# Kernel tuning notes

Hardware: AMD Instinct MI355X
Metric: run time of the kernel (lower is better)

## Reference

```python
import jax, jax.numpy as jnp
import numpy as np

EPS = 1e-6
WINDOW = 1024  # config.sliding_window; mask: causal AND (q_idx - kv_idx < WINDOW)


def rms_norm(x, w=None):
    y = x * jax.lax.rsqrt(jnp.mean(jnp.square(x), axis=-1, keepdims=True) + EPS)
    return y * w if w is not None else y


def rotate_half(x):
    x1, x2 = jnp.split(x, 2, axis=-1)
    return jnp.concatenate([-x2, x1], axis=-1)


def apply_rope(x, cos, sin):
    # x: [B,S,H,D], cos/sin: [B,S,D] -> unsqueeze head dim (rotary_dim == D, x_pass empty)
    cos = cos[:, :, None, :]
    sin = sin[:, :, None, :]
    return x * cos + rotate_half(x) * sin


def setup_inputs() -> dict:
    key = jax.random.key(0)
    ks = jax.random.split(key, 8)
    B, S, HID, NH, NKV, D = 1, 2048, 2560, 8, 4, 256
    scale = 0.02
    hidden_states = jax.random.normal(ks[0], (B, S, HID), dtype=jnp.float32)
    wq = jax.random.normal(ks[1], (HID, NH * D), dtype=jnp.float32) * scale
    wk = jax.random.normal(ks[2], (HID, NKV * D), dtype=jnp.float32) * scale
    wv = jax.random.normal(ks[3], (HID, NKV * D), dtype=jnp.float32) * scale
    wo = jax.random.normal(ks[4], (NH * D, HID), dtype=jnp.float32) * scale
    q_norm_w = jnp.ones((D,), dtype=jnp.float32)
    k_norm_w = jnp.ones((D,), dtype=jnp.float32)
    # standard RoPE tables, rotary_dim = head_dim
    pos = jnp.arange(S, dtype=jnp.float32)
    inv_freq = 1.0 / (10000.0 ** (jnp.arange(0, D, 2, dtype=jnp.float32) / D))
    freqs = pos[:, None] * inv_freq[None, :]           # [S, D/2]
    emb = jnp.concatenate([freqs, freqs], axis=-1)     # [S, D]
    cos = jnp.cos(emb)[None]                           # [1, S, D]
    sin = jnp.sin(emb)[None]
    return dict(hidden_states=hidden_states, cos=cos, sin=sin,
                wq=wq, wk=wk, wv=wv, wo=wo,
                q_norm_w=q_norm_w, k_norm_w=k_norm_w)


def reference(hidden_states, cos, sin, wq, wk, wv, wo, q_norm_w, k_norm_w):
    B, S, _ = hidden_states.shape
    D = q_norm_w.shape[0]
    # projections -> [B,S,H,D]
    q = (hidden_states @ wq).reshape(B, S, -1, D)
    k = (hidden_states @ wk).reshape(B, S, -1, D)
    v = (hidden_states @ wv).reshape(B, S, -1, D)
    # QK-norm then RoPE (v gets non-affine RMSNorm)
    q = apply_rope(rms_norm(q, q_norm_w), cos, sin)
    k = apply_rope(rms_norm(k, k_norm_w), cos, sin)
    v = rms_norm(v)
    NH, NKV = q.shape[2], k.shape[2]
    rep = NH // NKV  # GQA: repeat KV heads
    k = jnp.repeat(k, rep, axis=2)
    v = jnp.repeat(v, rep, axis=2)
    # attention with scale=1.0 (QK-norm replaces 1/sqrt(d))
    scores = jnp.einsum('bqhd,bkhd->bhqk', q, k)
    qi = jnp.arange(S)[:, None]
    ki = jnp.arange(S)[None, :]
    mask = (ki <= qi) & (qi - ki < WINDOW)  # causal sliding window
    scores = jnp.where(mask[None, None], scores, -jnp.inf)
    attn = jax.nn.softmax(scores, axis=-1)
    out = jnp.einsum('bhqk,bkhd->bqhd', attn, v).reshape(B, S, -1)
    return out @ wo
```

## Files before the change

kernel.cpp:

```cpp
#include <hip/hip_runtime.h>
#include <hip/hip_bf16.h>
#include <math.h>

#define S_LEN 2048
#define HID 2560
#define NH 8
#define NKV 4
#define HD 256
#define WINDOW 1024

typedef short short8 __attribute__((ext_vector_type(8)));
typedef short short4_t __attribute__((ext_vector_type(4)));
typedef float f32x4 __attribute__((ext_vector_type(4)));
typedef float float4_t __attribute__((ext_vector_type(4)));

__device__ __forceinline__ short bf16_rne(float x) {
  unsigned u = __float_as_uint(x);
  return (short)((u + 0x7FFFu + ((u >> 16) & 1u)) >> 16);
}
__device__ __forceinline__ void split2(float x, short &h, short &l) {
  unsigned u = __float_as_uint(x);
  unsigned hb = (u + 0x7FFFu + ((u >> 16) & 1u)) & 0xFFFF0000u;
  h = (short)(hb >> 16);
  float r = x - __uint_as_float(hb);
  l = bf16_rne(r);
}

__device__ __forceinline__ void gload16(const short* g, short* l) {
  __builtin_amdgcn_global_load_lds(
      (const __attribute__((address_space(1))) void*)g,
      (__attribute__((address_space(3))) void*)l, 16, 0, 0);
}

#define SWZ(g, r) ((((g) ^ ((r) & 7))) * 8)
template <int MODE>
__device__ __forceinline__ void gemm_body(
    const short* __restrict__ Ah, const short* __restrict__ Al,
    const short* __restrict__ Bh, const short* __restrict__ Bl,
    float* __restrict__ C, int K, int ldc, int m0, int n0, int tid,
    short (*__restrict__ Ahs)[64], short (*__restrict__ Als)[64],
    short (*__restrict__ Bhs)[64], short (*__restrict__ Bls)[64]) {
  constexpr bool USE_AL = (MODE & 1) != 0;
  constexpr bool USE_BL = (MODE & 2) != 0;
  const int wv = tid >> 6, lane = tid & 63;
  const int wm = (wv >> 1) * 32, wn = (wv & 1) * 64;
  const int quad = lane >> 4, col = lane & 15;
  const int lr = lane >> 3;
  const size_t lgofs = (size_t)(((lane & 7) ^ lr)) * 8;
  const size_t aBase = (size_t)(m0 + lr) * K + lgofs;
  const size_t bBase = (size_t)(n0 + lr) * K + lgofs;

  f32x4 acc[2][4];
#pragma unroll
  for (int i = 0; i < 2; i++)
#pragma unroll
    for (int j = 0; j < 4; j++) acc[i][j] = (f32x4){0.f, 0.f, 0.f, 0.f};

  for (int k0 = 0; k0 < K; k0 += 64) {
#pragma unroll
    for (int c = wv; c < 8; c += 4) {
      const size_t go = aBase + (size_t)c * 8 * K + k0;
      gload16(Ah + go, &Ahs[c * 8][0]);
      if (USE_AL) gload16(Al + go, &Als[c * 8][0]);
    }
#pragma unroll
    for (int c = wv; c < 16; c += 4) {
      const size_t go = bBase + (size_t)c * 8 * K + k0;
      gload16(Bh + go, &Bhs[c * 8][0]);
      if (USE_BL) gload16(Bl + go, &Bls[c * 8][0]);
    }
    __syncthreads();
#pragma unroll
    for (int ks = 0; ks < 2; ks++) {
      const int g = ks * 4 + quad;
      short8 afh[2], afl[2], bfh[4], bfl[4];
#pragma unroll
      for (int i = 0; i < 2; i++) {
        int ar = wm + i * 16 + col;
        afh[i] = *reinterpret_cast<const short8*>(&Ahs[ar][SWZ(g, ar)]);
        if (USE_AL)
          afl[i] = *reinterpret_cast<const short8*>(&Als[ar][SWZ(g, ar)]);
      }
#pragma unroll
      for (int j = 0; j < 4; j++) {
        int br = wn + j * 16 + col;
        bfh[j] = *reinterpret_cast<const short8*>(&Bhs[br][SWZ(g, br)]);
        if (USE_BL)
          bfl[j] = *reinterpret_cast<const short8*>(&Bls[br][SWZ(g, br)]);
      }
#pragma unroll
      for (int i = 0; i < 2; i++)
#pragma unroll
        for (int j = 0; j < 4; j++) {
          acc[i][j] = __builtin_amdgcn_mfma_f32_16x16x32_bf16(afh[i], bfh[j], acc[i][j], 0, 0, 0);
          if (USE_BL)
            acc[i][j] = __builtin_amdgcn_mfma_f32_16x16x32_bf16(afh[i], bfl[j], acc[i][j], 0, 0, 0);
          if (USE_AL)
            acc[i][j] = __builtin_amdgcn_mfma_f32_16x16x32_bf16(afl[i], bfh[j], acc[i][j], 0, 0, 0);
        }
    }
    __syncthreads();
  }
#pragma unroll
  for (int i = 0; i < 2; i++)
#pragma unroll
    for (int j = 0; j < 4; j++)
#pragma unroll
      for (int r = 0; r < 4; r++)
        C[(size_t)(m0 + wm + i * 16 + quad * 4 + r) * ldc + n0 + wn + j * 16 + col] =
            acc[i][j][r];
}

template <int MODE>
__global__ __launch_bounds__(256, 3)
void gemm_presplit(const short* __restrict__ Ah, const short* __restrict__ Al,
                   const short* __restrict__ Bh, const short* __restrict__ Bl,
                   float* __restrict__ C, int K, int ldc) {
  __shared__ short Ahs[64][64];
  __shared__ short Als[(MODE & 1) ? 64 : 1][64];
  __shared__ short Bhs[128][64];
  __shared__ short Bls[(MODE & 2) ? 128 : 1][64];
  gemm_body<MODE>(Ah, Al, Bh, Bl, C, K, ldc, blockIdx.y * 64, blockIdx.x * 128,
                  threadIdx.x, Ahs, Als, Bhs, Bls);
}

__global__ __launch_bounds__(256, 3)
void gemm_qkv(const short* __restrict__ Ah, const short* __restrict__ Al,
              const short* __restrict__ qkvTh, const short* __restrict__ qkvTl,
              float* __restrict__ Cqkv) {
  __shared__ short Ahs[64][64];
  __shared__ short Als[64][64];
  __shared__ short Bhs[128][64];
  __shared__ short Bls[128][64];
  const int b = blockIdx.x;
  if (b < 768) {
    gemm_body<3>(Ah, Al, qkvTh, qkvTl, Cqkv, HID, 4096, (b / 24) * 64,
                 (b % 24) * 128, threadIdx.x, Ahs, Als, Bhs, Bls);
  } else {
    const int t = b - 768;
    gemm_body<2>(Ah, Al, qkvTh + (size_t)3072 * HID, qkvTl + (size_t)3072 * HID,
                 Cqkv + 3072, HID, 4096, (t / 8) * 64, (t % 8) * 128,
                 threadIdx.x, Ahs, Als, Bhs, Bls);
  }
}

__device__ __forceinline__ void wsplitT_body(const float* __restrict__ W,
                                             short* __restrict__ WTh,
                                             short* __restrict__ WTl,
                                             int KW, int NW, int n_ofs,
                                             int k0, int n0, int tid,
                                             float (*T)[65]) {
  const int r = tid >> 4, c4 = (tid & 15) * 4;
#pragma unroll
  for (int p = 0; p < 4; p++) {
    float4_t v = *reinterpret_cast<const float4_t*>(
        &W[(size_t)(k0 + r + p * 16) * NW + n0 + c4]);
#pragma unroll
    for (int e = 0; e < 4; e++) T[r + p * 16][c4 + e] = v[e];
  }
  __syncthreads();
  const int gk = tid & 7;
#pragma unroll
  for (int pass = 0; pass < 2; pass++) {
    const int n_loc = (tid >> 3) + pass * 32;
    short8 hv, lv;
#pragma unroll
    for (int e = 0; e < 8; e++) {
      short hh, ll;
      split2(T[gk * 8 + e][n_loc], hh, ll);
      hv[e] = hh; lv[e] = ll;
    }
    size_t base = (size_t)(n_ofs + n0 + n_loc) * KW + k0 + gk * 8;
    *reinterpret_cast<short8*>(WTh + base) = hv;
    *reinterpret_cast<short8*>(WTl + base) = lv;
  }
}

__global__ __launch_bounds__(256)
void prep_kernel(const float* __restrict__ hs, const float* __restrict__ wq,
                 const float* __restrict__ wk, const float* __restrict__ wv,
                 const float* __restrict__ wo, short* __restrict__ Ah,
                 short* __restrict__ Al, short* __restrict__ qkvTh,
                 short* __restrict__ qkvTl, short* __restrict__ woTh,
                 short* __restrict__ woTl) {
  __shared__ float T[64][65];
  const int bx = blockIdx.x;
  const int tid = threadIdx.x;
  if (bx < 5120) {
    const int i = bx * 256 + tid;
    float4_t v = reinterpret_cast<const float4_t*>(hs)[i];
    short4_t h, l;
#pragma unroll
    for (int e = 0; e < 4; e++) {
      short hh, ll;
      split2(v[e], hh, ll);
      h[e] = hh; l[e] = ll;
    }
    reinterpret_cast<short4_t*>(Ah)[i] = h;
    reinterpret_cast<short4_t*>(Al)[i] = l;
  } else if (bx < 6400) {
    const int local = bx - 5120;
    wsplitT_body(wq, qkvTh, qkvTl, HID, 2048, 0, (local % 40) * 64,
                 (local / 40) * 64, tid, T);
  } else if (bx < 7040) {
    const int local = bx - 6400;
    wsplitT_body(wk, qkvTh, qkvTl, HID, 1024, 2048, (local % 40) * 64,
                 (local / 40) * 64, tid, T);
  } else if (bx < 7680) {
    const int local = bx - 7040;
    wsplitT_body(wv, qkvTh, qkvTl, HID, 1024, 3072, (local % 40) * 64,
                 (local / 40) * 64, tid, T);
  } else {
    const int local = bx - 7680;
    wsplitT_body(wo, woTh, woTl, 2048, HID, 0, (local % 32) * 64,
                 (local / 32) * 64, tid, T);
  }
}

__global__ __launch_bounds__(256)
void norm_kernel(const float* __restrict__ Cqkv, const float* __restrict__ kw,
                 const float* __restrict__ cosb, const float* __restrict__ sinb,
                 short* __restrict__ kh, short* __restrict__ kl,
                 short* __restrict__ vtb) {
  const int u = blockIdx.x & 7;
  const int sq = blockIdx.x >> 3;
  const int d = threadIdx.x;
  const int colbase = (u < 4) ? 2048 + u * HD : 3072 + (u - 4) * HD;
  const size_t idx = (size_t)sq * 4096 + colbase + d;
  float x = Cqkv[idx];
  float v = x * x;
#pragma unroll
  for (int off = 32; off; off >>= 1) v += __shfl_down(v, off);
  __shared__ float red[4];
  __shared__ float sscale;
  __shared__ float nb[HD];
  if ((d & 63) == 0) red[d >> 6] = v;
  __syncthreads();
  if (d == 0)
    sscale = rsqrtf((red[0] + red[1] + red[2] + red[3]) * (1.0f / HD) + 1e-6f);
  __syncthreads();
  if (u < 4) {
    float n = x * sscale * kw[d];
    nb[d] = n;
    __syncthreads();
    float other = (d < HD / 2) ? -nb[d + HD / 2] : nb[d - HD / 2];
    n = n * cosb[(size_t)sq * HD + d] + other * sinb[(size_t)sq * HD + d];
    short hh, ll;
    split2(n, hh, ll);
    const size_t b = ((size_t)sq * NKV + u) * HD + d;
    kh[b] = hh;
    kl[b] = ll;
  } else {
    vtb[((size_t)(u - 4) * HD + d) * S_LEN + sq] = bf16_rne(x * sscale);
  }
}

#define KSW(g, r) (((g) ^ ((r) & 7)) * 8)
#define VSW(g, d) ((((g) + ((d) >> 1)) & 3) * 8)
__global__ __launch_bounds__(256, 2)
void flash_attn2(const float* __restrict__ qn, int qrs,
                 const float* __restrict__ qw, const float* __restrict__ cosb,
                 const float* __restrict__ sinb,
                 const short* __restrict__ kh, const short* __restrict__ kl,
                 const short* __restrict__ vtb, float* __restrict__ oA,
                 float* __restrict__ oB, float* __restrict__ mlA,
                 float* __restrict__ mlB) {
  __shared__ short Kh[32][256], Kl[32][256];
  __shared__ short Vb[256][32];
  __shared__ short Ps[64][32];
  const int qt = blockIdx.x, h = blockIdx.y, sp = blockIdx.z;
  const int kvh = h >> 1;
  const int q0 = qt * 64;
  const int tid = threadIdx.x;
  const int w = tid >> 6, lane = tid & 63;
  const int quad = lane >> 4, col = lane & 15;
  float* oOut = sp ? oB : oA;
  float* mlOut = sp ? mlB : mlA;
  short8 qh[8], ql[8];
  {
    const int sq = q0 + w * 16 + col;
    const float* qrow = qn + (size_t)sq * qrs + h * HD;
    float xq[8][8];
    float ssum = 0.f;
#pragma unroll
    for (int s8 = 0; s8 < 8; s8++) {
      const int d0 = s8 * 32 + quad * 8;
      float4_t a = *reinterpret_cast<const float4_t*>(qrow + d0);
      float4_t b = *reinterpret_cast<const float4_t*>(qrow + d0 + 4);
#pragma unroll
      for (int e = 0; e < 4; e++) {
        xq[s8][e] = a[e];
        xq[s8][4 + e] = b[e];
        ssum += a[e] * a[e] + b[e] * b[e];
      }
    }
    ssum += __shfl_xor(ssum, 16);
    ssum += __shfl_xor(ssum, 32);
    const float scale = rsqrtf(ssum * (1.0f / HD) + 1e-6f);
#pragma unroll
    for (int s8 = 0; s8 < 8; s8++) {
      const int d0 = s8 * 32 + quad * 8;
      float4_t w0 = *reinterpret_cast<const float4_t*>(qw + d0);
      float4_t w1 = *reinterpret_cast<const float4_t*>(qw + d0 + 4);
#pragma unroll
      for (int e = 0; e < 4; e++) {
        xq[s8][e] *= scale * w0[e];
        xq[s8][4 + e] *= scale * w1[e];
      }
    }
    const float* crow = cosb + (size_t)sq * HD;
    const float* srow = sinb + (size_t)sq * HD;
#pragma unroll
    for (int s8 = 0; s8 < 8; s8++) {
      const int d0 = s8 * 32 + quad * 8;
      float4_t c0 = *reinterpret_cast<const float4_t*>(crow + d0);
      float4_t c1 = *reinterpret_cast<const float4_t*>(crow + d0 + 4);
      float4_t s0 = *reinterpret_cast<const float4_t*>(srow + d0);
      float4_t s1 = *reinterpret_cast<const float4_t*>(srow + d0 + 4);
      const float sgn = (s8 < 4) ? -1.f : 1.f;
      const int pp = s8 ^ 4;
#pragma unroll
      for (int e = 0; e < 4; e++) {
        short hh, ll;
        split2(xq[s8][e] * c0[e] + sgn * xq[pp][e] * s0[e], hh, ll);
        qh[s8][e] = hh; ql[s8][e] = ll;
        split2(xq[s8][4 + e] * c1[e] + sgn * xq[pp][4 + e] * s1[e], hh, ll);
        qh[s8][4 + e] = hh; ql[s8][4 + e] = ll;
      }
    }
  }
  f32x4 o[16];
#pragma unroll
  for (int i = 0; i < 16; i++) o[i] = (f32x4){0.f, 0.f, 0.f, 0.f};
  float m_r[4] = {-INFINITY, -INFINITY, -INFINITY, -INFINITY};
  float l_r[4] = {0.f, 0.f, 0.f, 0.f};
  const int lo_t = (q0 > 1023) ? ((q0 - 1023) >> 5) : 0;
  const int hi_t = (q0 + 63) >> 5;
  const int halfn = (hi_t - lo_t + 2) >> 1;
  const int t0 = sp ? (lo_t + halfn) : lo_t;
  const int t1 = sp ? hi_t : (lo_t + halfn - 1);
  for (int kt = t0; kt <= t1; kt++) {
    const int kt0 = kt << 5;
    __syncthreads();
#pragma unroll
    for (int i = 0; i < 4; i++) {
      int idx = tid + i * 256;
      int row = idx >> 5, g = idx & 31;
      size_t gofs = ((size_t)(kt0 + row) * NKV + kvh) * HD + g * 8;
      *reinterpret_cast<short8*>(&Kh[row][KSW(g, row)]) =
          *reinterpret_cast<const short8*>(kh + gofs);
      *reinterpret_cast<short8*>(&Kl[row][KSW(g, row)]) =
          *reinterpret_cast<const short8*>(kl + gofs);
    }
#pragma unroll
    for (int i = 0; i < 4; i++) {
      int idx = tid + i * 256;
      int d = idx >> 2, g = idx & 3;
      *reinterpret_cast<short8*>(&Vb[d][VSW(g, d)]) =
          *reinterpret_cast<const short8*>(
              vtb + ((size_t)kvh * HD + d) * S_LEN + kt0 + g * 8);
    }
    __syncthreads();
    f32x4 sc[2];
    sc[0] = (f32x4){0.f, 0.f, 0.f, 0.f};
    sc[1] = (f32x4){0.f, 0.f, 0.f, 0.f};
#pragma unroll
    for (int s8 = 0; s8 < 8; s8++) {
#pragma unroll
      for (int nt = 0; nt < 2; nt++) {
        const int br = nt * 16 + col;
        const short8 bh = *reinterpret_cast<const short8*>(
            &Kh[br][KSW(s8 * 4 + quad, br)]);
        const short8 bl = *reinterpret_cast<const short8*>(
            &Kl[br][KSW(s8 * 4 + quad, br)]);
        sc[nt] = __builtin_amdgcn_mfma_f32_16x16x32_bf16(qh[s8], bh, sc[nt], 0, 0, 0);
        sc[nt] = __builtin_amdgcn_mfma_f32_16x16x32_bf16(qh[s8], bl, sc[nt], 0, 0, 0);
        sc[nt] = __builtin_amdgcn_mfma_f32_16x16x32_bf16(ql[s8], bh, sc[nt], 0, 0, 0);
      }
    }
#pragma unroll
    for (int r = 0; r < 4; r++) {
      const int q_abs = q0 + w * 16 + quad * 4 + r;
      const int prow = w * 16 + quad * 4 + r;
#pragma unroll
      for (int nt = 0; nt < 2; nt++) {
        int k_abs = kt0 + nt * 16 + col;
        bool valid = (k_abs <= q_abs) && (q_abs - k_abs < WINDOW);
        if (!valid) sc[nt][r] = -INFINITY;
      }
      float mx = fmaxf(sc[0][r], sc[1][r]);
      mx = fmaxf(mx, __shfl_xor(mx, 1));
      mx = fmaxf(mx, __shfl_xor(mx, 2));
      mx = fmaxf(mx, __shfl_xor(mx, 4));
      mx = fmaxf(mx, __shfl_xor(mx, 8));
      float mn = fmaxf(m_r[r], mx);
      float alpha = (mn == -INFINITY) ? 1.f : __expf(m_r[r] - mn);
      m_r[r] = mn;
      float rsum = 0.f;
#pragma unroll
      for (int nt = 0; nt < 2; nt++) {
        float s = sc[nt][r];
        float e = (s == -INFINITY) ? 0.f : __expf(s - mn);
        rsum += e;
        int ge = nt * 2 + (col >> 3);
        Ps[prow][VSW(ge, prow) + (col & 7)] = bf16_rne(e);
      }
      rsum += __shfl_xor(rsum, 1);
      rsum += __shfl_xor(rsum, 2);
      rsum += __shfl_xor(rsum, 4);
      rsum += __shfl_xor(rsum, 8);
      l_r[r] = l_r[r] * alpha + rsum;
#pragma unroll
      for (int nt2 = 0; nt2 < 16; nt2++) o[nt2][r] *= alpha;
    }
    __syncthreads();
    {
      const int prow = w * 16 + col;
      const short8 pa = *reinterpret_cast<const short8*>(&Ps[prow][VSW(quad, prow)]);
#pragma unroll
      for (int nt = 0; nt < 16; nt++) {
        const int vr = nt * 16 + col;
        const short8 vb = *reinterpret_cast<const short8*>(&Vb[vr][VSW(quad, vr)]);
        o[nt] = __builtin_amdgcn_mfma_f32_16x16x32_bf16(pa, vb, o[nt], 0, 0, 0);
      }
    }
  }
#pragma unroll
  for (int r = 0; r < 4; r++) {
    const int row = q0 + w * 16 + quad * 4 + r;
    const size_t base = ((size_t)row * NH + h) * HD;
#pragma unroll
    for (int nt = 0; nt < 16; nt++) oOut[base + nt * 16 + col] = o[nt][r];
    if (col == 0) {
      mlOut[((size_t)row * NH + h) * 2] = m_r[r];
      mlOut[((size_t)row * NH + h) * 2 + 1] = l_r[r];
    }
  }
}

__global__ __launch_bounds__(256)
void combine_kernel(const float* __restrict__ oA, const float* __restrict__ oB,
                    const float* __restrict__ mlA, const float* __restrict__ mlB,
                    short* __restrict__ ctxh) {
  const int idx = blockIdx.x;
  const int d = threadIdx.x;
  const float mA = mlA[(size_t)idx * 2], lA = mlA[(size_t)idx * 2 + 1];
  const float mB = mlB[(size_t)idx * 2], lB = mlB[(size_t)idx * 2 + 1];
  const float m = fmaxf(mA, mB);
  const float eA = (mA == -INFINITY) ? 0.f : __expf(mA - m);
  const float eB = (mB == -INFINITY) ? 0.f : __expf(mB - m);
  const float inv = 1.0f / (eA * lA + eB * lB);
  const size_t b = (size_t)idx * HD + d;
  ctxh[b] = bf16_rne((eA * oA[b] + eB * oB[b]) * inv);
}

extern "C" void kernel_launch(void* const* d_in, const int* in_sizes, int n_in,
                              void* d_out, int out_size, void* d_ws, size_t ws_size,
                              hipStream_t stream) {
  const float* hs   = (const float*)d_in[0];
  const float* cosb = (const float*)d_in[1];
  const float* sinb = (const float*)d_in[2];
  const float* wq   = (const float*)d_in[3];
  const float* wk   = (const float*)d_in[4];
  const float* wv   = (const float*)d_in[5];
  const float* wo   = (const float*)d_in[6];
  const float* qw   = (const float*)d_in[7];
  const float* kw   = (const float*)d_in[8];
  dim3 blk(256);

  const size_t szAh   = (size_t)S_LEN * HID * 2;
  const size_t szQKVT = (size_t)4096 * HID * 2;
  const size_t szWoT  = (size_t)HID * 2048 * 2;
  const size_t szCqkv = (size_t)S_LEN * 4096 * 4;
  const size_t szKh   = (size_t)S_LEN * NKV * HD * 2;
  const size_t szMl   = (size_t)S_LEN * NH * 2 * 4;

  char* p = (char*)d_ws + 256;
  short* Ah    = (short*)p;  p += szAh;
  short* Al    = (short*)p;  p += szAh;
  short* qkvTh = (short*)p;  p += szQKVT;
  short* qkvTl = (short*)p;  p += szQKVT;
  short* woTh  = (short*)p;  p += szWoT;
  short* woTl  = (short*)p;  p += szWoT;
  float* Cqkv  = (float*)p;  p += szCqkv;
  short* kh    = (short*)p;  p += szKh;
  short* kl    = (short*)p;  p += szKh;
  short* vtb   = (short*)p;  p += szKh;
  float* mlA   = (float*)p;  p += szMl;
  float* mlB   = (float*)p;  p += szMl;
  float* oA    = (float*)Ah;
  float* oB    = (float*)d_out;
  short* ctxh  = qkvTh;

  prep_kernel<<<8960, blk, 0, stream>>>(hs, wq, wk, wv, wo, Ah, Al, qkvTh,
                                        qkvTl, woTh, woTl);
  gemm_qkv<<<1024, blk, 0, stream>>>(Ah, Al, qkvTh, qkvTl, Cqkv);
  norm_kernel<<<S_LEN * 8, blk, 0, stream>>>(Cqkv, kw, cosb, sinb, kh, kl, vtb);
  flash_attn2<<<dim3(S_LEN / 64, NH, 2), blk, 0, stream>>>(
      Cqkv, 4096, qw, cosb, sinb, kh, kl, vtb, oA, oB, mlA, mlB);
  combine_kernel<<<S_LEN * NH, blk, 0, stream>>>(oA, oB, mlA, mlB, ctxh);
  gemm_presplit<2><<<dim3(HID / 128, S_LEN / 64), blk, 0, stream>>>(
      ctxh, ctxh, woTh, woTl, (float*)d_out, 2048, HID);
}
```

Measured before the change: 417.4 us.

## Reorder QKV GEMM blocks, vectorize norm kernel, remap flash-attn block indices

The QKV GEMM now dispatches the cheaper V-projection blocks (single bf16 split) first and the heavier three-product blocks after them. The K/V norm kernel now processes one row per wavefront with float4 loads, a wave-level xor-shuffle reduction and shuffle-based rotate-half. This removes the block-wide syncthreads and shared memory it used before. The flash attention launch becomes a 1D grid with an index remap, so consecutive blocks spread across heads and splits rather than walking q tiles of one head, which is meant to improve load balance across compute units and L2 locality.

```diff
diff --git a/kernel.cpp b/kernel.cpp
--- a/kernel.cpp
+++ b/kernel.cpp
@@ -133,14 +133,14 @@
   __shared__ short Bhs[128][64];
   __shared__ short Bls[128][64];
   const int b = blockIdx.x;
-  if (b < 768) {
-    gemm_body<3>(Ah, Al, qkvTh, qkvTl, Cqkv, HID, 4096, (b / 24) * 64,
-                 (b % 24) * 128, threadIdx.x, Ahs, Als, Bhs, Bls);
+  if (b < 256) {
+    gemm_body<2>(Ah, Al, qkvTh + (size_t)3072 * HID, qkvTl + (size_t)3072 * HID,
+                 Cqkv + 3072, HID, 4096, (b / 8) * 64, (b % 8) * 128,
+                 threadIdx.x, Ahs, Als, Bhs, Bls);
   } else {
-    const int t = b - 768;
-    gemm_body<2>(Ah, Al, qkvTh + (size_t)3072 * HID, qkvTl + (size_t)3072 * HID,
-                 Cqkv + 3072, HID, 4096, (t / 8) * 64, (t % 8) * 128,
-                 threadIdx.x, Ahs, Als, Bhs, Bls);
+    const int t = b - 256;
+    gemm_body<3>(Ah, Al, qkvTh, qkvTl, Cqkv, HID, 4096, (t / 24) * 64,
+                 (t % 24) * 128, threadIdx.x, Ahs, Als, Bhs, Bls);
   }
 }
 
@@ -222,36 +222,43 @@
                  const float* __restrict__ cosb, const float* __restrict__ sinb,
                  short* __restrict__ kh, short* __restrict__ kl,
                  short* __restrict__ vtb) {
-  const int u = blockIdx.x & 7;
-  const int sq = blockIdx.x >> 3;
-  const int d = threadIdx.x;
+  const int unit = blockIdx.x * 4 + (threadIdx.x >> 6);
+  const int u = unit & 7;
+  const int sq = unit >> 3;
+  const int t = threadIdx.x & 63;
+  const int d = t * 4;
   const int colbase = (u < 4) ? 2048 + u * HD : 3072 + (u - 4) * HD;
-  const size_t idx = (size_t)sq * 4096 + colbase + d;
-  float x = Cqkv[idx];
-  float v = x * x;
-#pragma unroll
-  for (int off = 32; off; off >>= 1) v += __shfl_down(v, off);
-  __shared__ float red[4];
-  __shared__ float sscale;
-  __shared__ float nb[HD];
-  if ((d & 63) == 0) red[d >> 6] = v;
-  __syncthreads();
-  if (d == 0)
-    sscale = rsqrtf((red[0] + red[1] + red[2] + red[3]) * (1.0f / HD) + 1e-6f);
-  __syncthreads();
+  const float4_t x = *reinterpret_cast<const float4_t*>(
+      &Cqkv[(size_t)sq * 4096 + colbase + d]);
+  float v = x[0] * x[0] + x[1] * x[1] + x[2] * x[2] + x[3] * x[3];
+#pragma unroll
+  for (int off = 32; off; off >>= 1) v += __shfl_xor(v, off);
+  const float scale = rsqrtf(v * (1.0f / HD) + 1e-6f);
   if (u < 4) {
-    float n = x * sscale * kw[d];
-    nb[d] = n;
-    __syncthreads();
-    float other = (d < HD / 2) ? -nb[d + HD / 2] : nb[d - HD / 2];
-    n = n * cosb[(size_t)sq * HD + d] + other * sinb[(size_t)sq * HD + d];
-    short hh, ll;
-    split2(n, hh, ll);
+    const float4_t w = *reinterpret_cast<const float4_t*>(kw + d);
+    const float4_t cb = *reinterpret_cast<const float4_t*>(
+        &cosb[(size_t)sq * HD + d]);
+    const float4_t sb = *reinterpret_cast<const float4_t*>(
+        &sinb[(size_t)sq * HD + d]);
+    const float sgn = (t < 32) ? -1.f : 1.f;
+    short4_t hv, lv;
+#pragma unroll
+    for (int e = 0; e < 4; e++) {
+      const float n = x[e] * scale * w[e];
+      const float other = __shfl_xor(n, 32);
+      const float r = n * cb[e] + sgn * other * sb[e];
+      short hh, ll;
+      split2(r, hh, ll);
+      hv[e] = hh; lv[e] = ll;
+    }
     const size_t b = ((size_t)sq * NKV + u) * HD + d;
-    kh[b] = hh;
-    kl[b] = ll;
+    *reinterpret_cast<short4_t*>(kh + b) = hv;
+    *reinterpret_cast<short4_t*>(kl + b) = lv;
   } else {
-    vtb[((size_t)(u - 4) * HD + d) * S_LEN + sq] = bf16_rne(x * sscale);
+    const int hh = u - 4;
+#pragma unroll
+    for (int e = 0; e < 4; e++)
+      vtb[((size_t)hh * HD + d + e) * S_LEN + sq] = bf16_rne(x[e] * scale);
   }
 }
 
@@ -268,7 +275,8 @@
   __shared__ short Kh[32][256], Kl[32][256];
   __shared__ short Vb[256][32];
   __shared__ short Ps[64][32];
-  const int qt = blockIdx.x, h = blockIdx.y, sp = blockIdx.z;
+  const int wg = ((blockIdx.x & 7) << 6) + (blockIdx.x >> 3);
+  const int qt = wg & 31, h = (wg >> 5) & 7, sp = wg >> 8;
   const int kvh = h >> 1;
   const int q0 = qt * 64;
   const int tid = threadIdx.x;
@@ -495,8 +503,8 @@
   prep_kernel<<<8960, blk, 0, stream>>>(hs, wq, wk, wv, wo, Ah, Al, qkvTh,
                                         qkvTl, woTh, woTl);
   gemm_qkv<<<1024, blk, 0, stream>>>(Ah, Al, qkvTh, qkvTl, Cqkv);
-  norm_kernel<<<S_LEN * 8, blk, 0, stream>>>(Cqkv, kw, cosb, sinb, kh, kl, vtb);
-  flash_attn2<<<dim3(S_LEN / 64, NH, 2), blk, 0, stream>>>(
+  norm_kernel<<<4096, blk, 0, stream>>>(Cqkv, kw, cosb, sinb, kh, kl, vtb);
+  flash_attn2<<<512, blk, 0, stream>>>(
       Cqkv, 4096, qw, cosb, sinb, kh, kl, vtb, oA, oB, mlA, mlB);
   combine_kernel<<<S_LEN * NH, blk, 0, stream>>>(oA, oB, mlA, mlB, ctxh);
   gemm_presplit<2><<<dim3(HID / 128, S_LEN / 64), blk, 0, stream>>>(
```

Result: slower. 428.6 us (+2.7%).
